# Performance work log

Hardware: AMD Instinct MI355X
Metric: run time of the kernel (lower is better)

The kernel has to match this reference:

```python
import jax, jax.numpy as jnp
import numpy as np

N_TOP = 5  # self.n from __init__
EPS = 1e-10


def setup_inputs() -> dict:
    key = jax.random.key(0)
    k1, k2 = jax.random.split(key)
    support_set = jax.random.normal(k1, (8, 4096, 64), dtype=jnp.float32)
    query_set = jax.random.normal(k2, (8, 4096, 64), dtype=jnp.float32)
    return {"support_set": support_set, "query_set": query_set, "bshot": 2048}


def reference(support_set, query_set, bshot):
    # support_set: [B,S,D], query_set: [B,Q,D]
    sum_support = jnp.sum(support_set * support_set, axis=2)          # [B,S]
    support_magnitude = jax.lax.rsqrt(jnp.clip(sum_support, EPS))     # clamp(eps, inf).rsqrt()
    dot = jnp.einsum('bqd,bsd->bqs', query_set, support_set)          # [B,Q,S]
    cos = dot * support_magnitude[:, None, :]                         # scale per support column
    top_vals, _ = jax.lax.top_k(cos[:, :, :bshot], N_TOP)             # [B,Q,n]
    return jnp.concatenate([top_vals, cos[:, :, bshot:]], axis=2)     # [B,Q,n+(S-bshot)]
```

## Files before the change

kernel.cpp:

```cpp
#include <hip/hip_runtime.h>
#include <hip/hip_bf16.h>

#define B_ 8
#define S_ 4096
#define Q_ 4096
#define D_ 64

typedef __attribute__((ext_vector_type(8))) short short8;
typedef __attribute__((ext_vector_type(4))) float f32x4;

__device__ __forceinline__ unsigned short f2bf(float f) {
  union { float f; unsigned u; } v; v.f = f;
  unsigned u = v.u;
  u += 0x7FFFu + ((u >> 16) & 1u);
  return (unsigned short)(u >> 16);
}

__global__ void prep_kernel(const float* __restrict__ supp,
                            const float* __restrict__ query,
                            unsigned short* __restrict__ supp_bf,
                            unsigned short* __restrict__ query_bf) {
  int r = blockIdx.x * blockDim.x + threadIdx.x;
  const int nsupp = B_ * S_;
  const int total = nsupp + B_ * Q_;
  if (r >= total) return;
  const bool is_supp = r < nsupp;
  const float* src = is_supp ? (supp + (size_t)r * D_)
                             : (query + (size_t)(r - nsupp) * D_);
  unsigned short* dst = is_supp ? (supp_bf + (size_t)r * D_)
                                : (query_bf + (size_t)(r - nsupp) * D_);
  float4 v[D_ / 4];
  float sum = 0.f;
#pragma unroll
  for (int i = 0; i < D_ / 4; ++i) {
    v[i] = ((const float4*)src)[i];
    sum += v[i].x * v[i].x + v[i].y * v[i].y + v[i].z * v[i].z + v[i].w * v[i].w;
  }
  const float sc = is_supp ? rsqrtf(fmaxf(sum, 1e-10f)) : 1.0f;
#pragma unroll
  for (int i = 0; i < D_ / 4; ++i) {
    ushort4 h;
    h.x = f2bf(v[i].x * sc); h.y = f2bf(v[i].y * sc);
    h.z = f2bf(v[i].z * sc); h.w = f2bf(v[i].w * sc);
    ((ushort4*)dst)[i] = h;
  }
}

__device__ __forceinline__ void ins5(float (&t)[5], float v) {
  float a = v, b;
  b = fminf(t[0], a); t[0] = fmaxf(t[0], a); a = b;
  b = fminf(t[1], a); t[1] = fmaxf(t[1], a); a = b;
  b = fminf(t[2], a); t[2] = fmaxf(t[2], a); a = b;
  b = fminf(t[3], a); t[3] = fmaxf(t[3], a); a = b;
  t[4] = fmaxf(t[4], a);
}

__device__ __forceinline__ void lds_barrier() {
  asm volatile("s_waitcnt lgkmcnt(0)" ::: "memory");
  __builtin_amdgcn_s_barrier();
}

__global__ void cos_topk_kernel(const unsigned short* __restrict__ supp_bf,
                                const unsigned short* __restrict__ query_bf,
                                const int* __restrict__ pbshot,
                                float* __restrict__ out) {
  const int bs = *pbshot;
  const int OW = 5 + S_ - bs;

  const int b  = blockIdx.x >> 6;
  const int q0 = (blockIdx.x & 63) * 64;
  const int tid  = threadIdx.x;
  const int w    = tid >> 6;
  const int lane = tid & 63;
  const int l15  = lane & 15;
  const int l4   = lane >> 4;

  const int nt_top = bs >> 6;
  const int role = blockIdx.y;
  const bool is_top = (role == 0);
  int t0, t1;
  if (is_top) { t0 = 0; t1 = nt_top; }
  else {
    const int ct = (S_ >> 6) - nt_top;
    t0 = nt_top + (ct * (role - 1)) / 6;
    t1 = nt_top + (ct * role) / 6;
  }

  __shared__ unsigned short lds[2][64 * 64];
  __shared__ float elds[4][16][65];

  const int qrow = q0 + w * 16 + l15;
  const unsigned short* qbase = query_bf + (size_t)(b * Q_ + qrow) * D_;
  const short8 a0 = *(const short8*)(qbase + l4 * 8);
  const short8 a1 = *(const short8*)(qbase + 32 + l4 * 8);

  float tk[4][5];
#pragma unroll
  for (int r2 = 0; r2 < 4; ++r2)
#pragma unroll
    for (int j = 0; j < 5; ++j) tk[r2][j] = -INFINITY;

  const int srow  = tid >> 2;
  const int chunk = tid & 3;
  const unsigned short* gstage0 =
      supp_bf + ((size_t)b * S_ + srow) * D_ + chunk * 16;
  const int dsw0 = srow * 64 + ((chunk * 16 + 0) ^ ((srow & 7) << 3));
  const int dsw1 = srow * 64 + ((chunk * 16 + 8) ^ ((srow & 7) << 3));

  uint4 st0 = *(const uint4*)(gstage0 + (size_t)t0 * 64 * D_);
  uint4 st1 = *(const uint4*)(gstage0 + (size_t)t0 * 64 * D_ + 8);
  *(uint4*)&lds[0][dsw0] = st0;
  *(uint4*)&lds[0][dsw1] = st1;

  const int rbase = b * Q_ + q0 + w * 16 + l4 * 4;
  float* owave = out + (size_t)(b * Q_ + q0 + w * 16) * OW + 5 - bs;

  for (int t = t0; t < t1; ++t) {
    const int buf = (t - t0) & 1;
    if (t + 1 < t1) {
      const unsigned short* g = gstage0 + (size_t)(t + 1) * 64 * D_;
      st0 = *(const uint4*)(g);
      st1 = *(const uint4*)(g + 8);
    }
    lds_barrier();

    f32x4 ab[4];
#pragma unroll
    for (int fc = 0; fc < 4; ++fc) {
      const int scol = fc * 16 + l15;
      const int idx0 = scol * 64 + ((l4 * 8) ^ ((scol & 7) << 3));
      const int idx1 = scol * 64 + ((32 + l4 * 8) ^ ((scol & 7) << 3));
      const short8 b0 = *(const short8*)&lds[buf][idx0];
      const short8 b1 = *(const short8*)&lds[buf][idx1];
      f32x4 acc = {0.f, 0.f, 0.f, 0.f};
      acc = __builtin_amdgcn_mfma_f32_16x16x32_bf16(a0, b0, acc, 0, 0, 0);
      acc = __builtin_amdgcn_mfma_f32_16x16x32_bf16(a1, b1, acc, 0, 0, 0);

      if (is_top) {
#pragma unroll
        for (int r2 = 0; r2 < 4; ++r2) ins5(tk[r2], acc[r2]);
      } else {
        ab[fc] = acc;
      }
    }

    if (!is_top) {
#pragma unroll
      for (int fc = 0; fc < 4; ++fc)
#pragma unroll
        for (int r2 = 0; r2 < 4; ++r2)
          elds[w][l4 * 4 + r2][fc * 16 + l15] = ab[fc][r2];
#pragma unroll
      for (int i = 0; i < 16; ++i) {
        const float vv = elds[w][i][lane];
        owave[(size_t)i * OW + t * 64 + lane] = vv;
      }
    }

    if (t + 1 < t1) {
      *(uint4*)&lds[buf ^ 1][dsw0] = st0;
      *(uint4*)&lds[buf ^ 1][dsw1] = st1;
    }
  }

  if (is_top) {
#pragma unroll
    for (int m = 1; m <= 8; m <<= 1) {
#pragma unroll
      for (int r2 = 0; r2 < 4; ++r2) {
        float o0 = __shfl_xor(tk[r2][0], m);
        float o1 = __shfl_xor(tk[r2][1], m);
        float o2 = __shfl_xor(tk[r2][2], m);
        float o3 = __shfl_xor(tk[r2][3], m);
        float o4 = __shfl_xor(tk[r2][4], m);
        ins5(tk[r2], o0); ins5(tk[r2], o1); ins5(tk[r2], o2);
        ins5(tk[r2], o3); ins5(tk[r2], o4);
      }
    }
    if (l15 == 0) {
#pragma unroll
      for (int r2 = 0; r2 < 4; ++r2) {
        float* op = out + (size_t)(rbase + r2) * OW;
        op[0] = tk[r2][0]; op[1] = tk[r2][1]; op[2] = tk[r2][2];
        op[3] = tk[r2][3]; op[4] = tk[r2][4];
      }
    }
  }
}

extern "C" void kernel_launch(void* const* d_in, const int* in_sizes, int n_in,
                              void* d_out, int out_size, void* d_ws, size_t ws_size,
                              hipStream_t stream) {
  const float* supp  = (const float*)d_in[0];
  const float* query = (const float*)d_in[1];
  const int* pbshot  = (const int*)d_in[2];
  float* out = (float*)d_out;

  unsigned short* supp_bf  = (unsigned short*)d_ws;
  unsigned short* query_bf = supp_bf + (size_t)B_ * S_ * D_;

  const int rows = B_ * (S_ + Q_);
  prep_kernel<<<(rows + 255) / 256, 256, 0, stream>>>(supp, query, supp_bf,
                                                      query_bf);
  dim3 grid(B_ * (Q_ / 64), 7);
  cos_topk_kernel<<<grid, 256, 0, stream>>>(supp_bf, query_bf, pbshot, out);
}
```

Before: 84.79 us.

## Realign the non-top-k output stores to 128-byte boundaries using double-buffered LDS staging

Each output row has an odd width (OW), so the plain cos columns start at a different misalignment in every row. The non-top-k blocks now shift each row's store window so every wave writes a 32-float-aligned span. The stored values for a window are taken from two consecutive 64-column tiles kept in a double-buffered LDS staging area. The aim is to cut partial cache-line writes on the large output stream. The remainder tile count is hardcoded to 32, which assumes bshot = 2048, and the per-row staging adds more LDS traffic and index arithmetic.

```diff
diff --git a/kernel.cpp b/kernel.cpp
--- a/kernel.cpp
+++ b/kernel.cpp
@@ -66,6 +66,7 @@
                                 float* __restrict__ out) {
   const int bs = *pbshot;
   const int OW = 5 + S_ - bs;
+  const int RC = S_ - bs;
 
   const int b  = blockIdx.x >> 6;
   const int q0 = (blockIdx.x & 63) * 64;
@@ -78,27 +79,14 @@
   const int nt_top = bs >> 6;
   const int role = blockIdx.y;
   const bool is_top = (role == 0);
-  int t0, t1;
-  if (is_top) { t0 = 0; t1 = nt_top; }
-  else {
-    const int ct = (S_ >> 6) - nt_top;
-    t0 = nt_top + (ct * (role - 1)) / 6;
-    t1 = nt_top + (ct * role) / 6;
-  }
 
   __shared__ unsigned short lds[2][64 * 64];
-  __shared__ float elds[4][16][65];
+  __shared__ float elds[4][2][16][66];
 
   const int qrow = q0 + w * 16 + l15;
   const unsigned short* qbase = query_bf + (size_t)(b * Q_ + qrow) * D_;
   const short8 a0 = *(const short8*)(qbase + l4 * 8);
   const short8 a1 = *(const short8*)(qbase + 32 + l4 * 8);
-
-  float tk[4][5];
-#pragma unroll
-  for (int r2 = 0; r2 < 4; ++r2)
-#pragma unroll
-    for (int j = 0; j < 5; ++j) tk[r2][j] = -INFINITY;
 
   const int srow  = tid >> 2;
   const int chunk = tid & 3;
@@ -107,63 +95,47 @@
   const int dsw0 = srow * 64 + ((chunk * 16 + 0) ^ ((srow & 7) << 3));
   const int dsw1 = srow * 64 + ((chunk * 16 + 8) ^ ((srow & 7) << 3));
 
-  uint4 st0 = *(const uint4*)(gstage0 + (size_t)t0 * 64 * D_);
-  uint4 st1 = *(const uint4*)(gstage0 + (size_t)t0 * 64 * D_ + 8);
-  *(uint4*)&lds[0][dsw0] = st0;
-  *(uint4*)&lds[0][dsw1] = st1;
-
-  const int rbase = b * Q_ + q0 + w * 16 + l4 * 4;
-  float* owave = out + (size_t)(b * Q_ + q0 + w * 16) * OW + 5 - bs;
-
-  for (int t = t0; t < t1; ++t) {
-    const int buf = (t - t0) & 1;
-    if (t + 1 < t1) {
-      const unsigned short* g = gstage0 + (size_t)(t + 1) * 64 * D_;
-      st0 = *(const uint4*)(g);
-      st1 = *(const uint4*)(g + 8);
-    }
-    lds_barrier();
-
-    f32x4 ab[4];
-#pragma unroll
-    for (int fc = 0; fc < 4; ++fc) {
-      const int scol = fc * 16 + l15;
-      const int idx0 = scol * 64 + ((l4 * 8) ^ ((scol & 7) << 3));
-      const int idx1 = scol * 64 + ((32 + l4 * 8) ^ ((scol & 7) << 3));
-      const short8 b0 = *(const short8*)&lds[buf][idx0];
-      const short8 b1 = *(const short8*)&lds[buf][idx1];
-      f32x4 acc = {0.f, 0.f, 0.f, 0.f};
-      acc = __builtin_amdgcn_mfma_f32_16x16x32_bf16(a0, b0, acc, 0, 0, 0);
-      acc = __builtin_amdgcn_mfma_f32_16x16x32_bf16(a1, b1, acc, 0, 0, 0);
-
-      if (is_top) {
+  if (is_top) {
+    float tk[4][5];
+#pragma unroll
+    for (int r2 = 0; r2 < 4; ++r2)
+#pragma unroll
+      for (int j = 0; j < 5; ++j) tk[r2][j] = -INFINITY;
+
+    uint4 st0 = *(const uint4*)(gstage0);
+    uint4 st1 = *(const uint4*)(gstage0 + 8);
+    *(uint4*)&lds[0][dsw0] = st0;
+    *(uint4*)&lds[0][dsw1] = st1;
+
+    for (int t = 0; t < nt_top; ++t) {
+      const int buf = t & 1;
+      if (t + 1 < nt_top) {
+        const unsigned short* g = gstage0 + (size_t)(t + 1) * 64 * D_;
+        st0 = *(const uint4*)(g);
+        st1 = *(const uint4*)(g + 8);
+      }
+      lds_barrier();
+
+#pragma unroll
+      for (int fc = 0; fc < 4; ++fc) {
+        const int scol = fc * 16 + l15;
+        const int idx0 = scol * 64 + ((l4 * 8) ^ ((scol & 7) << 3));
+        const int idx1 = scol * 64 + ((32 + l4 * 8) ^ ((scol & 7) << 3));
+        const short8 b0 = *(const short8*)&lds[buf][idx0];
+        const short8 b1 = *(const short8*)&lds[buf][idx1];
+        f32x4 acc = {0.f, 0.f, 0.f, 0.f};
+        acc = __builtin_amdgcn_mfma_f32_16x16x32_bf16(a0, b0, acc, 0, 0, 0);
+        acc = __builtin_amdgcn_mfma_f32_16x16x32_bf16(a1, b1, acc, 0, 0, 0);
 #pragma unroll
         for (int r2 = 0; r2 < 4; ++r2) ins5(tk[r2], acc[r2]);
-      } else {
-        ab[fc] = acc;
-      }
-    }
-
-    if (!is_top) {
-#pragma unroll
-      for (int fc = 0; fc < 4; ++fc)
-#pragma unroll
-        for (int r2 = 0; r2 < 4; ++r2)
-          elds[w][l4 * 4 + r2][fc * 16 + l15] = ab[fc][r2];
-#pragma unroll
-      for (int i = 0; i < 16; ++i) {
-        const float vv = elds[w][i][lane];
-        owave[(size_t)i * OW + t * 64 + lane] = vv;
-      }
-    }
-
-    if (t + 1 < t1) {
-      *(uint4*)&lds[buf ^ 1][dsw0] = st0;
-      *(uint4*)&lds[buf ^ 1][dsw1] = st1;
-    }
-  }
-
-  if (is_top) {
+      }
+
+      if (t + 1 < nt_top) {
+        *(uint4*)&lds[buf ^ 1][dsw0] = st0;
+        *(uint4*)&lds[buf ^ 1][dsw1] = st1;
+      }
+    }
+
 #pragma unroll
     for (int m = 1; m <= 8; m <<= 1) {
 #pragma unroll
@@ -178,11 +150,71 @@
       }
     }
     if (l15 == 0) {
+      const int rbase = b * Q_ + q0 + w * 16 + l4 * 4;
 #pragma unroll
       for (int r2 = 0; r2 < 4; ++r2) {
         float* op = out + (size_t)(rbase + r2) * OW;
         op[0] = tk[r2][0]; op[1] = tk[r2][1]; op[2] = tk[r2][2];
         op[3] = tk[r2][3]; op[4] = tk[r2][4];
+      }
+    }
+  } else {
+    const int u0 = (32 * (role - 1)) / 6;
+    const int u1 = (32 * role) / 6;
+
+    {
+      const unsigned short* g = gstage0 + (size_t)(nt_top + u0) * 64 * D_;
+      uint4 s0 = *(const uint4*)(g);
+      uint4 s1 = *(const uint4*)(g + 8);
+      *(uint4*)&lds[0][dsw0] = s0;
+      *(uint4*)&lds[0][dsw1] = s1;
+    }
+    uint4 st0, st1;
+    for (int u = u0; u <= u1; ++u) {
+      const int p = (u - u0) & 1;
+      const bool pref = (u + 1 <= u1) && (u + 1 < 32);
+      if (pref) {
+        const unsigned short* g = gstage0 + (size_t)(nt_top + u + 1) * 64 * D_;
+        st0 = *(const uint4*)(g);
+        st1 = *(const uint4*)(g + 8);
+      }
+      lds_barrier();
+
+      if (u < 32) {
+#pragma unroll
+        for (int fc = 0; fc < 4; ++fc) {
+          const int scol = fc * 16 + l15;
+          const int idx0 = scol * 64 + ((l4 * 8) ^ ((scol & 7) << 3));
+          const int idx1 = scol * 64 + ((32 + l4 * 8) ^ ((scol & 7) << 3));
+          const short8 b0 = *(const short8*)&lds[p][idx0];
+          const short8 b1 = *(const short8*)&lds[p][idx1];
+          f32x4 acc = {0.f, 0.f, 0.f, 0.f};
+          acc = __builtin_amdgcn_mfma_f32_16x16x32_bf16(a0, b0, acc, 0, 0, 0);
+          acc = __builtin_amdgcn_mfma_f32_16x16x32_bf16(a1, b1, acc, 0, 0, 0);
+#pragma unroll
+          for (int r2 = 0; r2 < 4; ++r2)
+            elds[w][p][l4 * 4 + r2][fc * 16 + l15] = acc[r2];
+        }
+      }
+
+      if (u > u0 || u == 0) {
+#pragma unroll
+        for (int i = 0; i < 16; ++i) {
+          const int rw = b * Q_ + q0 + w * 16 + i;
+          const int c0 = (32 - ((rw * OW + 5) & 31)) & 31;
+          const int lc = c0 + lane;
+          const float vp = elds[w][p ^ 1][i][lc & 63];
+          const float vc = elds[w][p][i][lc & 63];
+          const float vv = (lc < 64) ? vp : vc;
+          const int col = u * 64 + c0 - 64 + lane;
+          if ((unsigned)col < (unsigned)RC)
+            out[(size_t)rw * OW + 5 + col] = vv;
+        }
+      }
+
+      if (pref) {
+        *(uint4*)&lds[p ^ 1][dsw0] = st0;
+        *(uint4*)&lds[p ^ 1][dsw1] = st1;
       }
     }
   }
```

Result: slower. 98.11 us (+15.7%).

## Split top-k region across four blocks with partial results and merge kernel

Applied to the files above, without the earlier changes.

The top-k column range, previously handled by a single block per query tile, is now split across four blocks. Each block writes a partial top-5 per row into a workspace buffer, and a new merge kernel combines the four partials into the final output. The copy region is now split four ways instead of six. This is meant to remove the load imbalance where the top-k block walked 32 tiles while the copy blocks walked about 5. It costs an extra kernel launch and a small round-trip through the partials buffer.

```diff
diff --git a/kernel.cpp b/kernel.cpp
--- a/kernel.cpp
+++ b/kernel.cpp
@@ -63,6 +63,7 @@
 __global__ void cos_topk_kernel(const unsigned short* __restrict__ supp_bf,
                                 const unsigned short* __restrict__ query_bf,
                                 const int* __restrict__ pbshot,
+                                float* __restrict__ partials,
                                 float* __restrict__ out) {
   const int bs = *pbshot;
   const int OW = 5 + S_ - bs;
@@ -76,14 +77,17 @@
   const int l4   = lane >> 4;
 
   const int nt_top = bs >> 6;
+  const int NT = S_ >> 6;
   const int role = blockIdx.y;
-  const bool is_top = (role == 0);
+  const bool is_top = (role < 4);
   int t0, t1;
-  if (is_top) { t0 = 0; t1 = nt_top; }
-  else {
-    const int ct = (S_ >> 6) - nt_top;
-    t0 = nt_top + (ct * (role - 1)) / 6;
-    t1 = nt_top + (ct * role) / 6;
+  if (is_top) {
+    t0 = (nt_top * role) / 4;
+    t1 = (nt_top * (role + 1)) / 4;
+  } else {
+    const int ct = NT - nt_top;
+    t0 = nt_top + (ct * (role - 4)) / 4;
+    t1 = nt_top + (ct * (role - 3)) / 4;
   }
 
   __shared__ unsigned short lds[2][64 * 64];
@@ -180,12 +184,27 @@
     if (l15 == 0) {
 #pragma unroll
       for (int r2 = 0; r2 < 4; ++r2) {
-        float* op = out + (size_t)(rbase + r2) * OW;
+        float* op = partials + (size_t)(rbase + r2) * 20 + role * 5;
         op[0] = tk[r2][0]; op[1] = tk[r2][1]; op[2] = tk[r2][2];
         op[3] = tk[r2][3]; op[4] = tk[r2][4];
       }
     }
   }
+}
+
+__global__ void topk_merge_kernel(const float* __restrict__ partials,
+                                  const int* __restrict__ pbshot,
+                                  float* __restrict__ out) {
+  const int bs = *pbshot;
+  const int OW = 5 + S_ - bs;
+  int r = blockIdx.x * blockDim.x + threadIdx.x;
+  if (r >= B_ * Q_) return;
+  const float* p = partials + (size_t)r * 20;
+  float tk[5] = {p[0], p[1], p[2], p[3], p[4]};
+#pragma unroll
+  for (int j = 5; j < 20; ++j) ins5(tk, p[j]);
+  float* op = out + (size_t)r * OW;
+  op[0] = tk[0]; op[1] = tk[1]; op[2] = tk[2]; op[3] = tk[3]; op[4] = tk[4];
 }
 
 extern "C" void kernel_launch(void* const* d_in, const int* in_sizes, int n_in,
@@ -198,10 +217,14 @@
 
   unsigned short* supp_bf  = (unsigned short*)d_ws;
   unsigned short* query_bf = supp_bf + (size_t)B_ * S_ * D_;
+  float* partials = (float*)(query_bf + (size_t)B_ * Q_ * D_);
 
   const int rows = B_ * (S_ + Q_);
   prep_kernel<<<(rows + 255) / 256, 256, 0, stream>>>(supp, query, supp_bf,
                                                       query_bf);
-  dim3 grid(B_ * (Q_ / 64), 7);
-  cos_topk_kernel<<<grid, 256, 0, stream>>>(supp_bf, query_bf, pbshot, out);
-}
+  dim3 grid(B_ * (Q_ / 64), 8);
+  cos_topk_kernel<<<grid, 256, 0, stream>>>(supp_bf, query_bf, pbshot,
+                                            partials, out);
+  topk_merge_kernel<<<(B_ * Q_ + 255) / 256, 256, 0, stream>>>(partials,
+                                                               pbshot, out);
+}
```

New measurement: 114.6 us. 35.2% more time.
